# Optimization experiments

Measured on AMD Instinct MI355X. Metric: run time of the kernel, lower is better.

The kernel has to match this reference:

```python
import jax, jax.numpy as jnp
import numpy as np

H = 16
N_JOBS = 1000000
N_MACH = 500000
NEG = -1e8

PARAM_SHAPES = [("jW1",(H,H)),("jb1",(H,)),("jW2",(H,H)),("jb2",(H,)),
                ("mW1",(H,H)),("mb1",(H,)),("mW2",(H,H)),("mb2",(H,)),
                ("aj_Wq",(H,H)),("aj_bq",(H,)),("aj_Wr",(H,H)),("aj_V",(H,)),
                ("am_Wq",(H,H)),("am_bq",(H,)),("am_Wr",(H,H)),("am_V",(H,)),
                ("ja_Wq",(H,H)),("ja_bq",(H,)),("ja_Wr",(H,H)),("ja_V",(H,)),
                ("ma_Wq",(H,H)),("ma_bq",(H,)),("ma_Wr",(H,H)),("ma_V",(H,)),
                ("g1W",(H,3*H)),("g1b",(H,)),("g2W",(H,3*H)),("g2b",(H,)),
                ("last_j",(H,))]

def setup_inputs() -> dict:
    key = jax.random.key(0)
    inp = {}
    inp["jobs"] = jax.random.normal(jax.random.fold_in(key, 0), (N_JOBS, H), dtype=jnp.float32)
    inp["machines"] = jax.random.normal(jax.random.fold_in(key, 1), (N_MACH, H), dtype=jnp.float32)
    inp["alloc_jobs_mask"] = jax.random.randint(jax.random.fold_in(key, 2), (N_JOBS,), 0, 2) > 0
    for i, (name, shape) in enumerate(PARAM_SHAPES):
        inp[name] = jax.random.normal(jax.random.fold_in(key, 10 + i), shape, dtype=jnp.float32) * 0.05
    return inp

def _emb(x, W1, b1, W2, b2):
    # custom_embedding: two tanh MLP layers (torch Linear: x @ W.T + b)
    h = jnp.tanh(x @ W1.T + b1)
    return jnp.tanh(h @ W2.T + b2)

def _att_logits(q, ref, Wq, bq, Wr, V):
    # Bahdanau additive attention: tanh(W_q q + W_r ref) @ V -> [S]
    return jnp.tanh((q @ Wq.T + bq) + ref @ Wr.T) @ V

def _query_att(q, ref, Wq, bq, Wr, V):
    # Attention with use_softmax=True followed by weighted sum over ref
    w = jax.nn.softmax(_att_logits(q, ref, Wq, bq, Wr, V))
    return w @ ref  # [H]

def reference(jobs, machines, alloc_jobs_mask,
              jW1, jb1, jW2, jb2, mW1, mb1, mW2, mb2,
              aj_Wq, aj_bq, aj_Wr, aj_V, am_Wq, am_bq, am_Wr, am_V,
              ja_Wq, ja_bq, ja_Wr, ja_V, ma_Wq, ma_bq, ma_Wr, ma_V,
              g1W, g1b, g2W, g2b, last_j):
    E_j = _emb(jobs, jW1, jb1, jW2, jb2)        # [Sj, H]
    E_m = _emb(machines, mW1, mb1, mW2, mb2)    # [Sm, H]

    # glimpse 1 conditioned on last_j
    g_j1 = _query_att(last_j, E_j, aj_Wq, aj_bq, aj_Wr, aj_V)
    g_m1 = _query_att(last_j, E_m, am_Wq, am_bq, am_Wr, am_V)
    g1 = jnp.tanh(jnp.concatenate([last_j, g_j1, g_m1]) @ g1W.T + g1b)

    # job pointer logits + invalid-action masking
    j_logits = _att_logits(g1, E_j, ja_Wq, ja_bq, ja_Wr, ja_V)
    j_logits = jnp.where(alloc_jobs_mask, j_logits, NEG)
    sel_j = jnp.argmax(j_logits)
    e_js = E_j[sel_j]

    # glimpse 2 conditioned on selected job embedding
    g_j2 = _query_att(e_js, E_j, aj_Wq, aj_bq, aj_Wr, aj_V)
    g_m2 = _query_att(e_js, E_m, am_Wq, am_bq, am_Wr, am_V)
    g2 = jnp.tanh(jnp.concatenate([e_js, g_j2, g_m2]) @ g2W.T + g2b)

    m_logits = _att_logits(g2, E_m, ma_Wq, ma_bq, ma_Wr, ma_V)
    sel_m = jnp.argmax(m_logits)

    logpas = jax.nn.log_softmax(j_logits)[sel_j] + jax.nn.log_softmax(m_logits)[sel_m]
    return sel_j, sel_m, logpas
```

## Files before the change

### kernel.cpp

```cpp
#include <hip/hip_runtime.h>
#include <cstddef>
#include <cstdint>


constexpr int NJ = 1000000;
constexpr int NM = 500000;
constexpr float NEGV = -1e8f;

constexpr int BLK = 256;
constexpr int ROWS_PER_BLK = 1024;
constexpr int GB_J = (NJ + ROWS_PER_BLK - 1) / ROWS_PER_BLK;
constexpr int GB_M = (NM + ROWS_PER_BLK - 1) / ROWS_PER_BLK;
constexpr int GB_TOT = GB_J + GB_M;
constexpr int EBLK = ROWS_PER_BLK * 16;

constexpr int S_QKJA = 0;
constexpr int S_QK2J = 16;
constexpr int S_QK2M = 32;
constexpr int S_EJS  = 48;
constexpr int S_QKMA = 64;
constexpr int S_LOGPJ = 80;
constexpr int S_SELJ  = 81;
constexpr int P1J = 128;
constexpr int P1M = P1J + GB_J * 17;
constexpr int P2V = P1M + GB_M * 17;
constexpr int P2I = P2V + GB_J;
constexpr int P2L = P2I + GB_J;
constexpr size_t E_OFF = 65536;
static_assert(P2L + GB_J <= (int)E_OFF, "partials overflow into E cache");
static_assert(NJ % 4 == 0 && NM % 4 == 0, "4-row packing needs n % 4 == 0");

typedef float v2f __attribute__((ext_vector_type(2)));

struct Params {
    const float *jobs, *machines;
    const int *mask;
    const float *jW1, *jb1, *jW2, *jb2;
    const float *mW1, *mb1, *mW2, *mb2;
    const float *aj_Wq, *aj_bq, *aj_Wr, *aj_V;
    const float *am_Wq, *am_bq, *am_Wr, *am_V;
    const float *ja_Wq, *ja_bq, *ja_Wr, *ja_V;
    const float *ma_Wq, *ma_bq, *ma_Wr, *ma_V;
    const float *g1W, *g1b, *g2W, *g2b, *last_j;
    float *S;
    float *Ej, *Em;
    float *out;
};


__device__ __forceinline__ float fast_tanh(float x) {
    float e = __builtin_amdgcn_exp2f(x * 2.8853900817779268f);
    float r = __builtin_amdgcn_rcpf(e + 1.0f);
    return fmaf(-2.0f, r, 1.0f);
}

__device__ __forceinline__ v2f vbc(float a) { v2f r; r.x = a; r.y = a; return r; }

__device__ __forceinline__ v2f vfma(float w, v2f b, v2f c) {
    return __builtin_elementwise_fma(vbc(w), b, c);
}
__device__ __forceinline__ v2f vfma2(v2f a, v2f b, v2f c) {
    return __builtin_elementwise_fma(a, b, c);
}
__device__ __forceinline__ v2f vtanh(v2f a) {
    v2f r; r.x = fast_tanh(a.x); r.y = fast_tanh(a.y); return r;
}

__device__ __forceinline__ void load16(const float* __restrict__ X, size_t r, float (&x)[16]) {
    const float4* p4 = reinterpret_cast<const float4*>(X) + r * 4;
    float4 a = p4[0], b = p4[1], c = p4[2], d = p4[3];
    x[0]=a.x; x[1]=a.y; x[2]=a.z; x[3]=a.w;
    x[4]=b.x; x[5]=b.y; x[6]=b.z; x[7]=b.w;
    x[8]=c.x; x[9]=c.y; x[10]=c.z; x[11]=c.w;
    x[12]=d.x; x[13]=d.y; x[14]=d.z; x[15]=d.w;
}

__device__ __forceinline__ void load16_v2(const float* __restrict__ X, size_t rA, size_t rB,
                                          v2f (&x)[16]) {
    float a[16], b[16];
    load16(X, rA, a);
    load16(X, rB, b);
#pragma unroll
    for (int k = 0; k < 16; ++k) { x[k].x = a[k]; x[k].y = b[k]; }
}

__device__ __forceinline__ void ecache_store4(float* __restrict__ Eb, int t,
                                              const v2f (&e0)[16], const v2f (&e1)[16]) {
    float4* p4 = reinterpret_cast<float4*>(Eb);
#pragma unroll
    for (int kp = 0; kp < 8; ++kp) {
        p4[kp * 512 + t]       = make_float4(e0[2*kp].x, e0[2*kp].y, e0[2*kp+1].x, e0[2*kp+1].y);
        p4[kp * 512 + 256 + t] = make_float4(e1[2*kp].x, e1[2*kp].y, e1[2*kp+1].x, e1[2*kp+1].y);
    }
}
__device__ __forceinline__ void ecache_load4(const float* __restrict__ Eb, int t,
                                             v2f (&e0)[16], v2f (&e1)[16]) {
    const float4* p4 = reinterpret_cast<const float4*>(Eb);
#pragma unroll
    for (int kp = 0; kp < 8; ++kp) {
        float4 q0 = p4[kp * 512 + t];
        float4 q1 = p4[kp * 512 + 256 + t];
        e0[2*kp].x = q0.x;   e0[2*kp].y = q0.y;
        e0[2*kp+1].x = q0.z; e0[2*kp+1].y = q0.w;
        e1[2*kp].x = q1.x;   e1[2*kp].y = q1.y;
        e1[2*kp+1].x = q1.z; e1[2*kp+1].y = q1.w;
    }
}

__device__ __forceinline__ void emb16_v2(const v2f (&x)[16],
                                         const float* __restrict__ W1, const float* __restrict__ b1,
                                         const float* __restrict__ W2, const float* __restrict__ b2,
                                         v2f (&e)[16]) {
    v2f h[16];
#pragma unroll
    for (int i = 0; i < 16; ++i) {
        v2f a = vbc(b1[i]);
#pragma unroll
        for (int k = 0; k < 16; ++k) a = vfma(W1[i * 16 + k], x[k], a);
        h[i] = vtanh(a);
    }
#pragma unroll
    for (int i = 0; i < 16; ++i) {
        v2f a = vbc(b2[i]);
#pragma unroll
        for (int k = 0; k < 16; ++k) a = vfma(W2[i * 16 + k], h[k], a);
        e[i] = vtanh(a);
    }
}

__device__ __forceinline__ v2f att_logit_v2(const v2f (&e)[16], const float (&qk)[16],
                                            const float* __restrict__ Wr,
                                            const float* __restrict__ V) {
    v2f acc = vbc(0.0f);
#pragma unroll
    for (int i = 0; i < 16; ++i) {
        v2f r = vbc(qk[i]);
#pragma unroll
        for (int k = 0; k < 16; ++k) r = vfma(Wr[i * 16 + k], e[k], r);
        acc = vfma2(vbc(V[i]), vtanh(r), acc);
    }
    return acc;
}

__device__ __forceinline__ float wave_reduce_sum(float v) {
#pragma unroll
    for (int off = 32; off > 0; off >>= 1) v += __shfl_xor(v, off, 64);
    return v;
}

__device__ __forceinline__ void wave_reduce_argmax(float &v, int &idx) {
#pragma unroll
    for (int off = 32; off > 0; off >>= 1) {
        float ov = __shfl_xor(v, off, 64);
        int oi = __shfl_xor(idx, off, 64);
        if (ov > v || (ov == v && oi < idx)) { v = ov; idx = oi; }
    }
}

__device__ __forceinline__ float block_sum(float v) {
    __shared__ float sm[4];
    v = wave_reduce_sum(v);
    __syncthreads();
    if ((threadIdx.x & 63) == 0) sm[threadIdx.x >> 6] = v;
    __syncthreads();
    return sm[0] + sm[1] + sm[2] + sm[3];
}

__device__ __forceinline__ void block_argmax(float &v, int &i) {
    __shared__ float sv[4];
    __shared__ int si[4];
    wave_reduce_argmax(v, i);
    __syncthreads();
    if ((threadIdx.x & 63) == 0) { sv[threadIdx.x >> 6] = v; si[threadIdx.x >> 6] = i; }
    __syncthreads();
    float bv = sv[0]; int bi = si[0];
#pragma unroll
    for (int k = 1; k < 4; ++k)
        if (sv[k] > bv || (sv[k] == bv && si[k] < bi)) { bv = sv[k]; bi = si[k]; }
    v = bv; i = bi;
}

__device__ __forceinline__ void block_sum17(float l, const float (&s)[16], float* dst) {
    const int lane = threadIdx.x & 63;
    float c[8];
#pragma unroll
    for (int j = 0; j < 8; ++j) {
        const bool hi = lane & 1;
        float t = __shfl_xor(hi ? s[j] : s[j + 8], 1, 64);
        c[j] = (hi ? s[j + 8] : s[j]) + t;
    }
    float d[4];
#pragma unroll
    for (int j = 0; j < 4; ++j) {
        const bool hi = lane & 2;
        float t = __shfl_xor(hi ? c[j] : c[j + 4], 2, 64);
        d[j] = (hi ? c[j + 4] : c[j]) + t;
    }
    float e2[2];
#pragma unroll
    for (int j = 0; j < 2; ++j) {
        const bool hi = lane & 4;
        float t = __shfl_xor(hi ? d[j] : d[j + 2], 4, 64);
        e2[j] = (hi ? d[j + 2] : d[j]) + t;
    }
    float f;
    {
        const bool hi = lane & 8;
        float t = __shfl_xor(hi ? e2[0] : e2[1], 8, 64);
        f = (hi ? e2[1] : e2[0]) + t;
    }
    f += __shfl_xor(f, 16, 64);
    f += __shfl_xor(f, 32, 64);
#pragma unroll
    for (int off = 32; off > 0; off >>= 1) l += __shfl_xor(l, off, 64);

    const int idx = ((lane & 1) << 3) | ((lane & 2) << 1) | ((lane & 4) >> 1) | ((lane & 8) >> 3);
    __shared__ float red[4][17];
    const int w = threadIdx.x >> 6;
    __syncthreads();
    if (lane < 16) red[w][1 + idx] = f;
    if (lane == 0) red[w][0] = l;
    __syncthreads();
    if (threadIdx.x < 17)
        dst[threadIdx.x] = red[0][threadIdx.x] + red[1][threadIdx.x] + red[2][threadIdx.x] + red[3][threadIdx.x];
}

__device__ __forceinline__ void wsum4(const v2f (&e0)[16], const v2f (&e1)[16],
                                      v2f w01, v2f w23, float (&s)[16]) {
#pragma unroll
    for (int i = 0; i < 16; ++i) {
        v2f t = vfma2(w23, e1[i], w01 * e0[i]);
        s[i] = t.x + t.y;
    }
}

template <bool CACHE>
__global__ __launch_bounds__(BLK) void k_emb_g1(Params p) {
    const bool isJob = blockIdx.x < GB_J;
    const float* X  = isJob ? p.jobs : p.machines;
    const float* W1 = isJob ? p.jW1 : p.mW1;
    const float* b1 = isJob ? p.jb1 : p.mb1;
    const float* W2 = isJob ? p.jW2 : p.mW2;
    const float* b2 = isJob ? p.jb2 : p.mb2;
    const float* Wr = isJob ? p.aj_Wr : p.am_Wr;
    const float* V  = isJob ? p.aj_V  : p.am_V;
    float* E = isJob ? p.Ej : p.Em;
    const int n  = isJob ? NJ : NM;
    const int b0 = isJob ? (int)blockIdx.x : (int)blockIdx.x - GB_J;

    const int r0 = b0 * ROWS_PER_BLK + 4 * (int)threadIdx.x;
    const bool v = r0 < n;
    const size_t a0 = v ? (size_t)r0 : 0;
    const size_t d  = v ? 1 : 0;

    v2f x0[16], x1[16];
    load16_v2(X, a0, a0 + d, x0);
    load16_v2(X, a0 + 2 * d, a0 + 3 * d, x1);

    __shared__ float qks[16];
    if (threadIdx.x < 16) {
        const float* Wq = isJob ? p.aj_Wq : p.am_Wq;
        const float* bq = isJob ? p.aj_bq : p.am_bq;
        const int i = threadIdx.x;
        float a = bq[i];
#pragma unroll
        for (int k = 0; k < 16; ++k) a = fmaf(Wq[i * 16 + k], p.last_j[k], a);
        qks[i] = a;
    }
    __syncthreads();
    float qk[16];
#pragma unroll
    for (int i = 0; i < 16; ++i) qk[i] = qks[i];

    v2f e0[16], e1[16];
    emb16_v2(x0, W1, b1, W2, b2, e0);
    emb16_v2(x1, W1, b1, W2, b2, e1);
    if (CACHE) ecache_store4(E + (size_t)b0 * EBLK, (int)threadIdx.x, e0, e1);
    v2f lg0 = att_logit_v2(e0, qk, Wr, V);
    v2f lg1 = att_logit_v2(e1, qk, Wr, V);
    v2f w01, w23;
    w01.x = v ? __expf(lg0.x) : 0.0f;
    w01.y = v ? __expf(lg0.y) : 0.0f;
    w23.x = v ? __expf(lg1.x) : 0.0f;
    w23.y = v ? __expf(lg1.y) : 0.0f;
    float l = (w01.x + w01.y) + (w23.x + w23.y);
    float s[16];
    wsum4(e0, e1, w01, w23, s);

    block_sum17(l, s, p.S + (isJob ? P1J : P1M) + (size_t)b0 * 17);
}

__global__ __launch_bounds__(BLK) void k_combine_g(Params p, int phase) {
    const float* PJ = p.S + P1J;
    const float* PM = p.S + P1M;
    float lJ = 0.0f, lM = 0.0f, sJ[16], sM[16];
#pragma unroll
    for (int c = 0; c < 16; ++c) { sJ[c] = 0.0f; sM[c] = 0.0f; }
    for (int i = threadIdx.x; i < GB_J; i += BLK) {
        lJ += PJ[i * 17];
#pragma unroll
        for (int c = 0; c < 16; ++c) sJ[c] += PJ[i * 17 + 1 + c];
    }
    for (int i = threadIdx.x; i < GB_M; i += BLK) {
        lM += PM[i * 17];
#pragma unroll
        for (int c = 0; c < 16; ++c) sM[c] += PM[i * 17 + 1 + c];
    }
    __shared__ float totJ[17], totM[17];
    block_sum17(lJ, sJ, totJ);
    block_sum17(lM, sM, totM);
    __syncthreads();

    __shared__ float cb[48], gbuf[16];
    if (threadIdx.x < 16) {
        int i = threadIdx.x;
        cb[i]      = phase ? p.S[S_EJS + i] : p.last_j[i];
        cb[16 + i] = totJ[1 + i] / totJ[0];
        cb[32 + i] = totM[1 + i] / totM[0];
    }
    __syncthreads();
    const float* gW  = phase ? p.g2W : p.g1W;
    const float* gbv = phase ? p.g2b : p.g1b;
    if (threadIdx.x < 16) {
        int i = threadIdx.x;
        float a = gbv[i];
#pragma unroll
        for (int k = 0; k < 48; ++k) a = fmaf(gW[i * 48 + k], cb[k], a);
        gbuf[i] = fast_tanh(a);
    }
    __syncthreads();
    const float* Wq = phase ? p.ma_Wq : p.ja_Wq;
    const float* bq = phase ? p.ma_bq : p.ja_bq;
    const int off = phase ? S_QKMA : S_QKJA;
    if (threadIdx.x < 16) {
        int i = threadIdx.x;
        float a = bq[i];
#pragma unroll
        for (int k = 0; k < 16; ++k) a = fmaf(Wq[i * 16 + k], gbuf[k], a);
        p.S[off + i] = a;
    }
}

template <bool CACHE>
__global__ __launch_bounds__(BLK) void k_jlogits(Params p) {
    const int r0 = blockIdx.x * ROWS_PER_BLK + 4 * (int)threadIdx.x;
    const bool v = r0 < NJ;
    const size_t a0 = v ? (size_t)r0 : 0;
    const size_t d  = v ? 1 : 0;

    v2f e0[16], e1[16];
    if (CACHE) {
        ecache_load4(p.Ej + (size_t)blockIdx.x * EBLK, (int)threadIdx.x, e0, e1);
    } else {
        v2f x0[16], x1[16];
        load16_v2(p.jobs, a0, a0 + d, x0);
        load16_v2(p.jobs, a0 + 2 * d, a0 + 3 * d, x1);
        emb16_v2(x0, p.jW1, p.jb1, p.jW2, p.jb2, e0);
        emb16_v2(x1, p.jW1, p.jb1, p.jW2, p.jb2, e1);
    }
    float qk[16];
#pragma unroll
    for (int i = 0; i < 16; ++i) qk[i] = p.S[S_QKJA + i];

    v2f lg0 = att_logit_v2(e0, qk, p.ja_Wr, p.ja_V);
    v2f lg1 = att_logit_v2(e1, qk, p.ja_Wr, p.ja_V);

    int4 mq = make_int4(0, 0, 0, 0);
    if (v) mq = *reinterpret_cast<const int4*>(p.mask + r0);
    const bool m0 = v && (mq.x != 0);
    const bool m1 = v && (mq.y != 0);
    const bool m2 = v && (mq.z != 0);
    const bool m3 = v && (mq.w != 0);
    float l = (m0 ? __expf(lg0.x) : 0.0f) + (m1 ? __expf(lg0.y) : 0.0f)
            + (m2 ? __expf(lg1.x) : 0.0f) + (m3 ? __expf(lg1.y) : 0.0f);
    float am0 = m0 ? lg0.x : NEGV - 1.0f;
    float am1 = m1 ? lg0.y : NEGV - 1.0f;
    float am2 = m2 ? lg1.x : NEGV - 1.0f;
    float am3 = m3 ? lg1.y : NEGV - 1.0f;
    float best = am0; int bi = r0;
    if (am1 > best) { best = am1; bi = r0 + 1; }
    if (am2 > best) { best = am2; bi = r0 + 2; }
    if (am3 > best) { best = am3; bi = r0 + 3; }

    l = wave_reduce_sum(l);
    wave_reduce_argmax(best, bi);
    __shared__ float rl[4], rv[4];
    __shared__ int ri[4];
    int w = threadIdx.x >> 6, ln = threadIdx.x & 63;
    if (ln == 0) { rl[w] = l; rv[w] = best; ri[w] = bi; }
    __syncthreads();
    if (threadIdx.x == 0) {
        float L = rl[0] + rl[1] + rl[2] + rl[3];
        float vv = rv[0]; int i = ri[0];
#pragma unroll
        for (int k = 1; k < 4; ++k)
            if (rv[k] > vv || (rv[k] == vv && ri[k] < i)) { vv = rv[k]; i = ri[k]; }
        p.S[P2V + blockIdx.x] = vv;
        p.S[P2I + blockIdx.x] = (float)i;
        p.S[P2L + blockIdx.x] = L;
    }
}

__global__ __launch_bounds__(BLK) void k_combine2(Params p) {
    float v = -3.4e38f; int vi = 0x7fffffff; float l = 0.0f;
    for (int i = threadIdx.x; i < GB_J; i += BLK) {
        float pv = p.S[P2V + i];
        int pi = (int)p.S[P2I + i];
        if (pv > v || (pv == v && pi < vi)) { v = pv; vi = pi; }
        l += p.S[P2L + i];
    }
    l = block_sum(l);
    block_argmax(v, vi);
    const int sel = vi;

    __shared__ float xb[16], hb[16], eb[16];
    if (threadIdx.x < 16) xb[threadIdx.x] = p.jobs[(size_t)sel * 16 + threadIdx.x];
    __syncthreads();
    if (threadIdx.x < 16) {
        int i = threadIdx.x;
        float a = p.jb1[i];
#pragma unroll
        for (int k = 0; k < 16; ++k) a = fmaf(p.jW1[i * 16 + k], xb[k], a);
        hb[i] = fast_tanh(a);
    }
    __syncthreads();
    if (threadIdx.x < 16) {
        int i = threadIdx.x;
        float a = p.jb2[i];
#pragma unroll
        for (int k = 0; k < 16; ++k) a = fmaf(p.jW2[i * 16 + k], hb[k], a);
        float e = fast_tanh(a);
        eb[i] = e;
        p.S[S_EJS + i] = e;
    }
    __syncthreads();
    if (threadIdx.x < 16) {
        int i = threadIdx.x;
        float a1 = p.aj_bq[i], a2 = p.am_bq[i];
#pragma unroll
        for (int k = 0; k < 16; ++k) {
            a1 = fmaf(p.aj_Wq[i * 16 + k], eb[k], a1);
            a2 = fmaf(p.am_Wq[i * 16 + k], eb[k], a2);
        }
        p.S[S_QK2J + i] = a1;
        p.S[S_QK2M + i] = a2;
    }
    if (threadIdx.x == 0) {
        p.S[S_LOGPJ] = v - logf(l);
        p.S[S_SELJ] = (float)sel;
    }
}

template <bool CACHE>
__global__ __launch_bounds__(BLK) void k_glimpse2(Params p) {
    const bool isJob = blockIdx.x < GB_J;
    const float* Wr = isJob ? p.aj_Wr : p.am_Wr;
    const float* V  = isJob ? p.aj_V  : p.am_V;
    const float* E  = isJob ? p.Ej : p.Em;
    const float* X  = isJob ? p.jobs : p.machines;
    const float* W1 = isJob ? p.jW1 : p.mW1;
    const float* b1 = isJob ? p.jb1 : p.mb1;
    const float* W2 = isJob ? p.jW2 : p.mW2;
    const float* b2 = isJob ? p.jb2 : p.mb2;
    const int n  = isJob ? NJ : NM;
    const int b0 = isJob ? (int)blockIdx.x : (int)blockIdx.x - GB_J;
    const int qoff = isJob ? S_QK2J : S_QK2M;

    const int r0 = b0 * ROWS_PER_BLK + 4 * (int)threadIdx.x;
    const bool v = r0 < n;
    const size_t a0 = v ? (size_t)r0 : 0;
    const size_t d  = v ? 1 : 0;

    v2f e0[16], e1[16];
    if (CACHE) {
        ecache_load4(E + (size_t)b0 * EBLK, (int)threadIdx.x, e0, e1);
    } else {
        v2f x0[16], x1[16];
        load16_v2(X, a0, a0 + d, x0);
        load16_v2(X, a0 + 2 * d, a0 + 3 * d, x1);
        emb16_v2(x0, W1, b1, W2, b2, e0);
        emb16_v2(x1, W1, b1, W2, b2, e1);
    }
    float qk[16];
#pragma unroll
    for (int i = 0; i < 16; ++i) qk[i] = p.S[qoff + i];

    v2f lg0 = att_logit_v2(e0, qk, Wr, V);
    v2f lg1 = att_logit_v2(e1, qk, Wr, V);
    v2f w01, w23;
    w01.x = v ? __expf(lg0.x) : 0.0f;
    w01.y = v ? __expf(lg0.y) : 0.0f;
    w23.x = v ? __expf(lg1.x) : 0.0f;
    w23.y = v ? __expf(lg1.y) : 0.0f;
    float l = (w01.x + w01.y) + (w23.x + w23.y);
    float s[16];
    wsum4(e0, e1, w01, w23, s);

    block_sum17(l, s, p.S + (isJob ? P1J : P1M) + (size_t)b0 * 17);
}

template <bool CACHE>
__global__ __launch_bounds__(BLK) void k_mlogits(Params p) {
    const int r0 = blockIdx.x * ROWS_PER_BLK + 4 * (int)threadIdx.x;
    const bool v = r0 < NM;
    const size_t a0 = v ? (size_t)r0 : 0;
    const size_t d  = v ? 1 : 0;

    v2f e0[16], e1[16];
    if (CACHE) {
        ecache_load4(p.Em + (size_t)blockIdx.x * EBLK, (int)threadIdx.x, e0, e1);
    } else {
        v2f x0[16], x1[16];
        load16_v2(p.machines, a0, a0 + d, x0);
        load16_v2(p.machines, a0 + 2 * d, a0 + 3 * d, x1);
        emb16_v2(x0, p.mW1, p.mb1, p.mW2, p.mb2, e0);
        emb16_v2(x1, p.mW1, p.mb1, p.mW2, p.mb2, e1);
    }
    float qk[16];
#pragma unroll
    for (int i = 0; i < 16; ++i) qk[i] = p.S[S_QKMA + i];

    v2f lg0 = att_logit_v2(e0, qk, p.ma_Wr, p.ma_V);
    v2f lg1 = att_logit_v2(e1, qk, p.ma_Wr, p.ma_V);
    float l = (v ? __expf(lg0.x) : 0.0f) + (v ? __expf(lg0.y) : 0.0f)
            + (v ? __expf(lg1.x) : 0.0f) + (v ? __expf(lg1.y) : 0.0f);
    float am0 = v ? lg0.x : -3.4e38f;
    float am1 = v ? lg0.y : -3.4e38f;
    float am2 = v ? lg1.x : -3.4e38f;
    float am3 = v ? lg1.y : -3.4e38f;
    float best = am0; int bi = r0;
    if (am1 > best) { best = am1; bi = r0 + 1; }
    if (am2 > best) { best = am2; bi = r0 + 2; }
    if (am3 > best) { best = am3; bi = r0 + 3; }

    l = wave_reduce_sum(l);
    wave_reduce_argmax(best, bi);
    __shared__ float rl[4], rv[4];
    __shared__ int ri[4];
    int w = threadIdx.x >> 6, ln = threadIdx.x & 63;
    if (ln == 0) { rl[w] = l; rv[w] = best; ri[w] = bi; }
    __syncthreads();
    if (threadIdx.x == 0) {
        float L = rl[0] + rl[1] + rl[2] + rl[3];
        float vv = rv[0]; int i = ri[0];
#pragma unroll
        for (int k = 1; k < 4; ++k)
            if (rv[k] > vv || (rv[k] == vv && ri[k] < i)) { vv = rv[k]; i = ri[k]; }
        p.S[P2V + blockIdx.x] = vv;
        p.S[P2I + blockIdx.x] = (float)i;
        p.S[P2L + blockIdx.x] = L;
    }
}

__global__ __launch_bounds__(BLK) void k_combine4(Params p) {
    float v = -3.4e38f; int vi = 0x7fffffff; float l = 0.0f;
    for (int i = threadIdx.x; i < GB_M; i += BLK) {
        float pv = p.S[P2V + i];
        int pi = (int)p.S[P2I + i];
        if (pv > v || (pv == v && pi < vi)) { v = pv; vi = pi; }
        l += p.S[P2L + i];
    }
    l = block_sum(l);
    block_argmax(v, vi);
    if (threadIdx.x == 0) {
        p.out[0] = p.S[S_SELJ];
        p.out[1] = (float)vi;
        p.out[2] = p.S[S_LOGPJ] + (v - logf(l));
    }
}

extern "C" void kernel_launch(void* const* d_in, const int* in_sizes, int n_in,
                              void* d_out, int out_size, void* d_ws, size_t ws_size,
                              hipStream_t stream) {
    Params p;
    p.jobs     = (const float*)d_in[0];
    p.machines = (const float*)d_in[1];
    p.mask     = (const int*)d_in[2];
    p.jW1 = (const float*)d_in[3];  p.jb1 = (const float*)d_in[4];
    p.jW2 = (const float*)d_in[5];  p.jb2 = (const float*)d_in[6];
    p.mW1 = (const float*)d_in[7];  p.mb1 = (const float*)d_in[8];
    p.mW2 = (const float*)d_in[9];  p.mb2 = (const float*)d_in[10];
    p.aj_Wq = (const float*)d_in[11]; p.aj_bq = (const float*)d_in[12];
    p.aj_Wr = (const float*)d_in[13]; p.aj_V  = (const float*)d_in[14];
    p.am_Wq = (const float*)d_in[15]; p.am_bq = (const float*)d_in[16];
    p.am_Wr = (const float*)d_in[17]; p.am_V  = (const float*)d_in[18];
    p.ja_Wq = (const float*)d_in[19]; p.ja_bq = (const float*)d_in[20];
    p.ja_Wr = (const float*)d_in[21]; p.ja_V  = (const float*)d_in[22];
    p.ma_Wq = (const float*)d_in[23]; p.ma_bq = (const float*)d_in[24];
    p.ma_Wr = (const float*)d_in[25]; p.ma_V  = (const float*)d_in[26];
    p.g1W = (const float*)d_in[27]; p.g1b = (const float*)d_in[28];
    p.g2W = (const float*)d_in[29]; p.g2b = (const float*)d_in[30];
    p.last_j = (const float*)d_in[31];
    p.S = (float*)d_ws;
    p.Ej = (float*)d_ws + E_OFF;
    p.Em = p.Ej + (size_t)GB_J * EBLK;
    p.out = (float*)d_out;

    const size_t needed = (E_OFF + (size_t)GB_TOT * EBLK) * sizeof(float);
    const bool cache = ws_size >= needed;

    if (cache) {
        k_emb_g1<true><<<GB_TOT, BLK, 0, stream>>>(p);
        k_combine_g<<<1, BLK, 0, stream>>>(p, 0);
        k_jlogits<true><<<GB_J, BLK, 0, stream>>>(p);
        k_combine2<<<1, BLK, 0, stream>>>(p);
        k_glimpse2<true><<<GB_TOT, BLK, 0, stream>>>(p);
        k_combine_g<<<1, BLK, 0, stream>>>(p, 1);
        k_mlogits<true><<<GB_M, BLK, 0, stream>>>(p);
        k_combine4<<<1, BLK, 0, stream>>>(p);
    } else {
        k_emb_g1<false><<<GB_TOT, BLK, 0, stream>>>(p);
        k_combine_g<<<1, BLK, 0, stream>>>(p, 0);
        k_jlogits<false><<<GB_J, BLK, 0, stream>>>(p);
        k_combine2<<<1, BLK, 0, stream>>>(p);
        k_glimpse2<false><<<GB_TOT, BLK, 0, stream>>>(p);
        k_combine_g<<<1, BLK, 0, stream>>>(p, 1);
        k_mlogits<false><<<GB_M, BLK, 0, stream>>>(p);
        k_combine4<<<1, BLK, 0, stream>>>(p);
    }
}
```

Measured before the change: 286.9 us.

## Fold single-block combine kernels into consumer kernels via redundant per-block reduction

Removes the three single-block combine launches by having every block of the following large kernel redo the partial reduction itself (glimpse combine, job argmax selection and embedding), keeping the results in shared memory. The aim is to drop the launch gaps and serialization of tiny one-block kernels between the big passes. In exchange, each of roughly a thousand blocks rereads all partials (about 1.5k x 17 floats, plus the argmax partials) and does redundant small matvecs before starting its main work. The machine-logit partials move to their own buffer so they no longer overwrite the job partials that every block of the machine-logit kernel still reads.

```diff
diff --git a/kernel.cpp b/kernel.cpp
--- a/kernel.cpp
+++ b/kernel.cpp
@@ -14,11 +14,6 @@
 constexpr int GB_TOT = GB_J + GB_M;
 constexpr int EBLK = ROWS_PER_BLK * 16;
 
-constexpr int S_QKJA = 0;
-constexpr int S_QK2J = 16;
-constexpr int S_QK2M = 32;
-constexpr int S_EJS  = 48;
-constexpr int S_QKMA = 64;
 constexpr int S_LOGPJ = 80;
 constexpr int S_SELJ  = 81;
 constexpr int P1J = 128;
@@ -26,8 +21,11 @@
 constexpr int P2V = P1M + GB_M * 17;
 constexpr int P2I = P2V + GB_J;
 constexpr int P2L = P2I + GB_J;
+constexpr int P3V = P2L + GB_J;
+constexpr int P3I = P3V + GB_M;
+constexpr int P3L = P3I + GB_M;
 constexpr size_t E_OFF = 65536;
-static_assert(P2L + GB_J <= (int)E_OFF, "partials overflow into E cache");
+static_assert(P3L + GB_M <= (int)E_OFF, "partials overflow into E cache");
 static_assert(NJ % 4 == 0 && NM % 4 == 0, "4-row packing needs n % 4 == 0");
 
 typedef float v2f __attribute__((ext_vector_type(2)));
@@ -234,6 +232,96 @@
     }
 }
 
+
+__device__ __forceinline__ void combine_g_to(const Params& p, int phase,
+                                             const float* cvec, float* qkout) {
+    const float* PJ = p.S + P1J;
+    const float* PM = p.S + P1M;
+    float lJ = 0.0f, lM = 0.0f, sJ[16], sM[16];
+#pragma unroll
+    for (int c = 0; c < 16; ++c) { sJ[c] = 0.0f; sM[c] = 0.0f; }
+    for (int i = threadIdx.x; i < GB_J; i += BLK) {
+        lJ += PJ[i * 17];
+#pragma unroll
+        for (int c = 0; c < 16; ++c) sJ[c] += PJ[i * 17 + 1 + c];
+    }
+    for (int i = threadIdx.x; i < GB_M; i += BLK) {
+        lM += PM[i * 17];
+#pragma unroll
+        for (int c = 0; c < 16; ++c) sM[c] += PM[i * 17 + 1 + c];
+    }
+    __shared__ float totJ[17], totM[17];
+    block_sum17(lJ, sJ, totJ);
+    block_sum17(lM, sM, totM);
+    __syncthreads();
+
+    __shared__ float cb[48], gbuf[16];
+    if (threadIdx.x < 16) {
+        int i = threadIdx.x;
+        cb[i]      = cvec[i];
+        cb[16 + i] = totJ[1 + i] / totJ[0];
+        cb[32 + i] = totM[1 + i] / totM[0];
+    }
+    __syncthreads();
+    const float* gW  = phase ? p.g2W : p.g1W;
+    const float* gbv = phase ? p.g2b : p.g1b;
+    if (threadIdx.x < 16) {
+        int i = threadIdx.x;
+        float a = gbv[i];
+#pragma unroll
+        for (int k = 0; k < 48; ++k) a = fmaf(gW[i * 48 + k], cb[k], a);
+        gbuf[i] = fast_tanh(a);
+    }
+    __syncthreads();
+    const float* Wq = phase ? p.ma_Wq : p.ja_Wq;
+    const float* bq = phase ? p.ma_bq : p.ja_bq;
+    if (threadIdx.x < 16) {
+        int i = threadIdx.x;
+        float a = bq[i];
+#pragma unroll
+        for (int k = 0; k < 16; ++k) a = fmaf(Wq[i * 16 + k], gbuf[k], a);
+        qkout[i] = a;
+    }
+    __syncthreads();
+}
+
+__device__ __forceinline__ void select_job(const Params& p, float* eb, bool writeLogp) {
+    float v = -3.4e38f; int vi = 0x7fffffff; float l = 0.0f;
+    for (int i = threadIdx.x; i < GB_J; i += BLK) {
+        float pv = p.S[P2V + i];
+        int pi = (int)p.S[P2I + i];
+        if (pv > v || (pv == v && pi < vi)) { v = pv; vi = pi; }
+        l += p.S[P2L + i];
+    }
+    l = block_sum(l);
+    block_argmax(v, vi);
+    const int sel = vi;
+
+    __shared__ float xb[16], hb[16];
+    if (threadIdx.x < 16) xb[threadIdx.x] = p.jobs[(size_t)sel * 16 + threadIdx.x];
+    __syncthreads();
+    if (threadIdx.x < 16) {
+        int i = threadIdx.x;
+        float a = p.jb1[i];
+#pragma unroll
+        for (int k = 0; k < 16; ++k) a = fmaf(p.jW1[i * 16 + k], xb[k], a);
+        hb[i] = fast_tanh(a);
+    }
+    __syncthreads();
+    if (threadIdx.x < 16) {
+        int i = threadIdx.x;
+        float a = p.jb2[i];
+#pragma unroll
+        for (int k = 0; k < 16; ++k) a = fmaf(p.jW2[i * 16 + k], hb[k], a);
+        eb[i] = fast_tanh(a);
+    }
+    if (writeLogp && threadIdx.x == 0) {
+        p.S[S_LOGPJ] = v - logf(l);
+        p.S[S_SELJ] = (float)sel;
+    }
+    __syncthreads();
+}
+
 template <bool CACHE>
 __global__ __launch_bounds__(BLK) void k_emb_g1(Params p) {
     const bool isJob = blockIdx.x < GB_J;
@@ -290,59 +378,11 @@
     block_sum17(l, s, p.S + (isJob ? P1J : P1M) + (size_t)b0 * 17);
 }
 
-__global__ __launch_bounds__(BLK) void k_combine_g(Params p, int phase) {
-    const float* PJ = p.S + P1J;
-    const float* PM = p.S + P1M;
-    float lJ = 0.0f, lM = 0.0f, sJ[16], sM[16];
-#pragma unroll
-    for (int c = 0; c < 16; ++c) { sJ[c] = 0.0f; sM[c] = 0.0f; }
-    for (int i = threadIdx.x; i < GB_J; i += BLK) {
-        lJ += PJ[i * 17];
-#pragma unroll
-        for (int c = 0; c < 16; ++c) sJ[c] += PJ[i * 17 + 1 + c];
-    }
-    for (int i = threadIdx.x; i < GB_M; i += BLK) {
-        lM += PM[i * 17];
-#pragma unroll
-        for (int c = 0; c < 16; ++c) sM[c] += PM[i * 17 + 1 + c];
-    }
-    __shared__ float totJ[17], totM[17];
-    block_sum17(lJ, sJ, totJ);
-    block_sum17(lM, sM, totM);
-    __syncthreads();
-
-    __shared__ float cb[48], gbuf[16];
-    if (threadIdx.x < 16) {
-        int i = threadIdx.x;
-        cb[i]      = phase ? p.S[S_EJS + i] : p.last_j[i];
-        cb[16 + i] = totJ[1 + i] / totJ[0];
-        cb[32 + i] = totM[1 + i] / totM[0];
-    }
-    __syncthreads();
-    const float* gW  = phase ? p.g2W : p.g1W;
-    const float* gbv = phase ? p.g2b : p.g1b;
-    if (threadIdx.x < 16) {
-        int i = threadIdx.x;
-        float a = gbv[i];
-#pragma unroll
-        for (int k = 0; k < 48; ++k) a = fmaf(gW[i * 48 + k], cb[k], a);
-        gbuf[i] = fast_tanh(a);
-    }
-    __syncthreads();
-    const float* Wq = phase ? p.ma_Wq : p.ja_Wq;
-    const float* bq = phase ? p.ma_bq : p.ja_bq;
-    const int off = phase ? S_QKMA : S_QKJA;
-    if (threadIdx.x < 16) {
-        int i = threadIdx.x;
-        float a = bq[i];
-#pragma unroll
-        for (int k = 0; k < 16; ++k) a = fmaf(Wq[i * 16 + k], gbuf[k], a);
-        p.S[off + i] = a;
-    }
-}
-
 template <bool CACHE>
 __global__ __launch_bounds__(BLK) void k_jlogits(Params p) {
+    __shared__ float qkja[16];
+    combine_g_to(p, 0, p.last_j, qkja);
+
     const int r0 = blockIdx.x * ROWS_PER_BLK + 4 * (int)threadIdx.x;
     const bool v = r0 < NJ;
     const size_t a0 = v ? (size_t)r0 : 0;
@@ -360,7 +400,7 @@
     }
     float qk[16];
 #pragma unroll
-    for (int i = 0; i < 16; ++i) qk[i] = p.S[S_QKJA + i];
+    for (int i = 0; i < 16; ++i) qk[i] = qkja[i];
 
     v2f lg0 = att_logit_v2(e0, qk, p.ja_Wr, p.ja_V);
     v2f lg1 = att_logit_v2(e1, qk, p.ja_Wr, p.ja_V);
@@ -401,39 +441,10 @@
     }
 }
 
-__global__ __launch_bounds__(BLK) void k_combine2(Params p) {
-    float v = -3.4e38f; int vi = 0x7fffffff; float l = 0.0f;
-    for (int i = threadIdx.x; i < GB_J; i += BLK) {
-        float pv = p.S[P2V + i];
-        int pi = (int)p.S[P2I + i];
-        if (pv > v || (pv == v && pi < vi)) { v = pv; vi = pi; }
-        l += p.S[P2L + i];
-    }
-    l = block_sum(l);
-    block_argmax(v, vi);
-    const int sel = vi;
-
-    __shared__ float xb[16], hb[16], eb[16];
-    if (threadIdx.x < 16) xb[threadIdx.x] = p.jobs[(size_t)sel * 16 + threadIdx.x];
-    __syncthreads();
-    if (threadIdx.x < 16) {
-        int i = threadIdx.x;
-        float a = p.jb1[i];
-#pragma unroll
-        for (int k = 0; k < 16; ++k) a = fmaf(p.jW1[i * 16 + k], xb[k], a);
-        hb[i] = fast_tanh(a);
-    }
-    __syncthreads();
-    if (threadIdx.x < 16) {
-        int i = threadIdx.x;
-        float a = p.jb2[i];
-#pragma unroll
-        for (int k = 0; k < 16; ++k) a = fmaf(p.jW2[i * 16 + k], hb[k], a);
-        float e = fast_tanh(a);
-        eb[i] = e;
-        p.S[S_EJS + i] = e;
-    }
-    __syncthreads();
+template <bool CACHE>
+__global__ __launch_bounds__(BLK) void k_glimpse2(Params p) {
+    __shared__ float eb[16], q2[32];
+    select_job(p, eb, false);
     if (threadIdx.x < 16) {
         int i = threadIdx.x;
         float a1 = p.aj_bq[i], a2 = p.am_bq[i];
@@ -442,17 +453,11 @@
             a1 = fmaf(p.aj_Wq[i * 16 + k], eb[k], a1);
             a2 = fmaf(p.am_Wq[i * 16 + k], eb[k], a2);
         }
-        p.S[S_QK2J + i] = a1;
-        p.S[S_QK2M + i] = a2;
-    }
-    if (threadIdx.x == 0) {
-        p.S[S_LOGPJ] = v - logf(l);
-        p.S[S_SELJ] = (float)sel;
-    }
-}
-
-template <bool CACHE>
-__global__ __launch_bounds__(BLK) void k_glimpse2(Params p) {
+        q2[i] = a1;
+        q2[16 + i] = a2;
+    }
+    __syncthreads();
+
     const bool isJob = blockIdx.x < GB_J;
     const float* Wr = isJob ? p.aj_Wr : p.am_Wr;
     const float* V  = isJob ? p.aj_V  : p.am_V;
@@ -464,7 +469,13 @@
     const float* b2 = isJob ? p.jb2 : p.mb2;
     const int n  = isJob ? NJ : NM;
     const int b0 = isJob ? (int)blockIdx.x : (int)blockIdx.x - GB_J;
-    const int qoff = isJob ? S_QK2J : S_QK2M;
+
+    float qk[16];
+    {
+        const float* qsrc = q2 + (isJob ? 0 : 16);
+#pragma unroll
+        for (int i = 0; i < 16; ++i) qk[i] = qsrc[i];
+    }
 
     const int r0 = b0 * ROWS_PER_BLK + 4 * (int)threadIdx.x;
     const bool v = r0 < n;
@@ -481,10 +492,6 @@
         emb16_v2(x0, W1, b1, W2, b2, e0);
         emb16_v2(x1, W1, b1, W2, b2, e1);
     }
-    float qk[16];
-#pragma unroll
-    for (int i = 0; i < 16; ++i) qk[i] = p.S[qoff + i];
-
     v2f lg0 = att_logit_v2(e0, qk, Wr, V);
     v2f lg1 = att_logit_v2(e1, qk, Wr, V);
     v2f w01, w23;
@@ -501,6 +508,10 @@
 
 template <bool CACHE>
 __global__ __launch_bounds__(BLK) void k_mlogits(Params p) {
+    __shared__ float eb[16], qkma[16];
+    select_job(p, eb, true);
+    combine_g_to(p, 1, eb, qkma);
+
     const int r0 = blockIdx.x * ROWS_PER_BLK + 4 * (int)threadIdx.x;
     const bool v = r0 < NM;
     const size_t a0 = v ? (size_t)r0 : 0;
@@ -518,7 +529,7 @@
     }
     float qk[16];
 #pragma unroll
-    for (int i = 0; i < 16; ++i) qk[i] = p.S[S_QKMA + i];
+    for (int i = 0; i < 16; ++i) qk[i] = qkma[i];
 
     v2f lg0 = att_logit_v2(e0, qk, p.ma_Wr, p.ma_V);
     v2f lg1 = att_logit_v2(e1, qk, p.ma_Wr, p.ma_V);
@@ -546,19 +557,19 @@
 #pragma unroll
         for (int k = 1; k < 4; ++k)
             if (rv[k] > vv || (rv[k] == vv && ri[k] < i)) { vv = rv[k]; i = ri[k]; }
-        p.S[P2V + blockIdx.x] = vv;
-        p.S[P2I + blockIdx.x] = (float)i;
-        p.S[P2L + blockIdx.x] = L;
+        p.S[P3V + blockIdx.x] = vv;
+        p.S[P3I + blockIdx.x] = (float)i;
+        p.S[P3L + blockIdx.x] = L;
     }
 }
 
 __global__ __launch_bounds__(BLK) void k_combine4(Params p) {
     float v = -3.4e38f; int vi = 0x7fffffff; float l = 0.0f;
     for (int i = threadIdx.x; i < GB_M; i += BLK) {
-        float pv = p.S[P2V + i];
-        int pi = (int)p.S[P2I + i];
+        float pv = p.S[P3V + i];
+        int pi = (int)p.S[P3I + i];
         if (pv > v || (pv == v && pi < vi)) { v = pv; vi = pi; }
-        l += p.S[P2L + i];
+        l += p.S[P3L + i];
     }
     l = block_sum(l);
     block_argmax(v, vi);
@@ -601,20 +612,14 @@
 
     if (cache) {
         k_emb_g1<true><<<GB_TOT, BLK, 0, stream>>>(p);
-        k_combine_g<<<1, BLK, 0, stream>>>(p, 0);
         k_jlogits<true><<<GB_J, BLK, 0, stream>>>(p);
-        k_combine2<<<1, BLK, 0, stream>>>(p);
         k_glimpse2<true><<<GB_TOT, BLK, 0, stream>>>(p);
-        k_combine_g<<<1, BLK, 0, stream>>>(p, 1);
         k_mlogits<true><<<GB_M, BLK, 0, stream>>>(p);
         k_combine4<<<1, BLK, 0, stream>>>(p);
     } else {
         k_emb_g1<false><<<GB_TOT, BLK, 0, stream>>>(p);
-        k_combine_g<<<1, BLK, 0, stream>>>(p, 0);
         k_jlogits<false><<<GB_J, BLK, 0, stream>>>(p);
-        k_combine2<<<1, BLK, 0, stream>>>(p);
         k_glimpse2<false><<<GB_TOT, BLK, 0, stream>>>(p);
-        k_combine_g<<<1, BLK, 0, stream>>>(p, 1);
         k_mlogits<false><<<GB_M, BLK, 0, stream>>>(p);
         k_combine4<<<1, BLK, 0, stream>>>(p);
     }
```

New measurement: 310.3 us. 1.08x slower.
